# Kernel tuning notes

Hardware: AMD Instinct MI355X
Metric: run time of the kernel (lower is better)

The kernel has to match this reference:

```python
import jax, jax.numpy as jnp
import numpy as np

N_NODES = 100000
N_EDGES = 800000
D_NODE = 64          # node_channels
D_EDGE = 4           # edge_feature_dim (2*layer_idx+2, layer 1)
H_MSG = 128          # message_hidden_channels
H_UPD = 128          # update_hidden_channels


def setup_inputs() -> dict:
    key = jax.random.key(0)
    ks = jax.random.split(key, 9)
    s = 0.05  # small init scale for numerical stability
    return {
        "x": jax.random.normal(ks[0], (N_NODES, D_NODE), dtype=jnp.float32),
        "edge_index": jax.random.randint(ks[1], (2, N_EDGES), 0, N_NODES, dtype=jnp.int32),
        "edge_features": jax.random.uniform(ks[2], (N_EDGES, D_EDGE), dtype=jnp.float32),
        "W1": jax.random.normal(ks[3], (2 * D_NODE + D_EDGE, H_MSG), dtype=jnp.float32) * s,
        "b1": jnp.zeros((H_MSG,), dtype=jnp.float32),
        "W2": jax.random.normal(ks[4], (H_MSG, D_NODE), dtype=jnp.float32) * s,
        "b2": jnp.zeros((D_NODE,), dtype=jnp.float32),
        "U1": jax.random.normal(ks[5], (2 * D_NODE, H_UPD), dtype=jnp.float32) * s,
        "bu1": jnp.zeros((H_UPD,), dtype=jnp.float32),
        "U2": jax.random.normal(ks[6], (H_UPD, D_NODE), dtype=jnp.float32) * s,
        "bu2": jnp.zeros((D_NODE,), dtype=jnp.float32),
    }


def reference(x, edge_index, edge_features, W1, b1, W2, b2, U1, bu1, U2, bu2):
    src, dst = edge_index[0], edge_index[1]
    # message phase: gather endpoints, log1p edge feats, concat, 2-layer MLP
    ef = jnp.log1p(edge_features)                       # [E, D_EDGE]
    msg_in = jnp.concatenate([x[src], x[dst], ef], axis=-1)  # [E, 2D+De]
    messages = jax.nn.relu(msg_in @ W1 + b1) @ W2 + b2  # [E, D_NODE]
    # aggregate: scatter-add into destination nodes
    agg = jnp.zeros_like(x).at[dst].add(messages)       # [N, D_NODE]
    # update phase
    upd_in = jnp.concatenate([x, agg], axis=-1)         # [N, 2*D_NODE]
    return jax.nn.relu(upd_in @ U1 + bu1) @ U2 + bu2    # [N, D_NODE]
```

## Files before the change

### kernel.cpp

```cpp
#include <hip/hip_runtime.h>
#include <math.h>

#define NN 100000
#define NE 800000
#define DN 64
#define DE 4
#define HH 128
#define NT 64
#define NT2 64
#define SCAN_B 256
#define NBLK_SCAN ((NN + SCAN_B - 1) / SCAN_B)
#define EPAD 16
#define AGG_BLOCKS 2048

using bf16x8 = __attribute__((ext_vector_type(8))) short;
using f32x4  = __attribute__((ext_vector_type(4))) float;

__device__ __forceinline__ unsigned short f2bf(float f) {
    unsigned int u = __float_as_uint(f);
    unsigned int r = (u + 0x7fffu + ((u >> 16) & 1u)) >> 16;
    return (unsigned short)r;
}
__device__ __forceinline__ float bf2f(unsigned short h) {
    return __uint_as_float(((unsigned int)h) << 16);
}
__device__ __forceinline__ float2 bfpair2f(unsigned int v) {
    return make_float2(__uint_as_float(v << 16),
                       __uint_as_float(v & 0xffff0000u));
}
__device__ __forceinline__ int rfl_i(int v) { return __builtin_amdgcn_readfirstlane(v); }

__global__ __launch_bounds__(256) void k_xproj(const float* __restrict__ x,
                                               const unsigned short* __restrict__ Wpx,
                                               unsigned short* __restrict__ XAb,
                                               float* __restrict__ XB) {
    __shared__ unsigned short sA[8 * 64 * 8];
    const int n0 = blockIdx.x * NT;
    const int t  = threadIdx.x;
    const int w    = t >> 6;
    const int l    = t & 63;
    const int quad = l >> 4;
    const int l16  = l & 15;

#pragma unroll
    for (int it = 0; it < 4; ++it) {
        const int flat = t + it * 256;
        const int node = flat >> 4;
        const int c    = flat & 15;
        const int gn   = n0 + node;
        float4 v = make_float4(0.f, 0.f, 0.f, 0.f);
        if (gn < NN) v = *(const float4*)(x + (size_t)gn * DN + c * 4);
        const int k = c * 4, Q = k >> 3, j0 = k & 7;
        uint2 pk;
        pk.x = (unsigned)f2bf(v.x) | ((unsigned)f2bf(v.y) << 16);
        pk.y = (unsigned)f2bf(v.z) | ((unsigned)f2bf(v.w) << 16);
        *(uint2*)(&sA[(Q * 64 + node) * 8 + j0]) = pk;
    }
    __syncthreads();

    const int mrow = w * 16 + l16;
    f32x4 acc[16];
#pragma unroll
    for (int nt = 0; nt < 16; ++nt) { acc[nt][0] = 0.f; acc[nt][1] = 0.f; acc[nt][2] = 0.f; acc[nt][3] = 0.f; }

#pragma unroll
    for (int kb = 0; kb < 2; ++kb) {
        bf16x8 a = *(const bf16x8*)(const void*)(&sA[((kb * 4 + quad) * 64 + mrow) * 8]);
#pragma unroll
        for (int nt = 0; nt < 16; ++nt) {
            bf16x8 b = *(const bf16x8*)(const void*)(Wpx + ((size_t)(nt * 2 + kb) * 64 + l) * 8);
            acc[nt] = __builtin_amdgcn_mfma_f32_16x16x32_bf16(a, b, acc[nt], 0, 0, 0);
        }
    }
#pragma unroll
    for (int nt = 0; nt < 8; ++nt) {
        const int col = nt * 16 + l16;
#pragma unroll
        for (int r = 0; r < 4; ++r) {
            const int gn = n0 + w * 16 + quad * 4 + r;
            if (gn < NN) XAb[(size_t)gn * HH + col] = f2bf(acc[nt][r]);
        }
    }
#pragma unroll
    for (int nt = 8; nt < 16; ++nt) {
        const int col = (nt - 8) * 16 + l16;
#pragma unroll
        for (int r = 0; r < 4; ++r) {
            const int gn = n0 + w * 16 + quad * 4 + r;
            if (gn < NN) XB[(size_t)gn * HH + col] = acc[nt][r];
        }
    }
}

__global__ __launch_bounds__(256) void k_fold(const float* __restrict__ W2,
                                              const float* __restrict__ U1,
                                              const float* __restrict__ b2,
                                              float* __restrict__ Wc,
                                              float* __restrict__ cvec) {
    const int idx = blockIdx.x * 256 + threadIdx.x;
    const float* u1b = U1 + (size_t)DN * HH;
    if (blockIdx.x < 64) {
        const int r = idx >> 7;
        const int c = idx & 127;
        float acc = 0.f;
#pragma unroll 8
        for (int j = 0; j < DN; ++j)
            acc = fmaf(W2[(size_t)r * DN + j], u1b[(size_t)j * HH + c], acc);
        Wc[(size_t)r * HH + c] = acc;
    } else if (threadIdx.x < HH) {
        const int c = threadIdx.x;
        float acc = 0.f;
#pragma unroll 8
        for (int j = 0; j < DN; ++j)
            acc = fmaf(b2[j], u1b[(size_t)j * HH + c], acc);
        cvec[c] = acc;
    }
}

__global__ __launch_bounds__(256) void k_pack(const float* __restrict__ U1,
                                              const float* __restrict__ Wc,
                                              const float* __restrict__ U2,
                                              const float* __restrict__ W1,
                                              unsigned short* __restrict__ Wpa,
                                              unsigned short* __restrict__ Wpb,
                                              unsigned short* __restrict__ Wpx) {
    const int tid = blockIdx.x * 256 + threadIdx.x;
    if (tid < 3072) {
        const int l  = tid & 63;
        const int kb = (tid >> 6) % 6;
        const int n  = tid / 384;
        const int kbase = kb * 32 + (l >> 4) * 8;
        const int col   = n * 16 + (l & 15);
        unsigned short tmp[8];
#pragma unroll
        for (int j = 0; j < 8; ++j) {
            const int k = kbase + j;
            const float v = (k < DN) ? U1[(size_t)k * HH + col]
                                     : Wc[(size_t)(k - DN) * HH + col];
            tmp[j] = f2bf(v);
        }
        *(uint4*)(Wpa + (size_t)tid * 8) = *(const uint4*)tmp;
    } else if (tid < 4096) {
        const int t2 = tid - 3072;
        const int l  = t2 & 63;
        const int kb = (t2 >> 6) & 3;
        const int n2 = t2 >> 8;
        const int kbase = kb * 32 + (l >> 4) * 8;
        const int col   = n2 * 16 + (l & 15);
        unsigned short tmp[8];
#pragma unroll
        for (int j = 0; j < 8; ++j) tmp[j] = f2bf(U2[(size_t)(kbase + j) * DN + col]);
        *(uint4*)(Wpb + (size_t)t2 * 8) = *(const uint4*)tmp;
    } else if (tid < 6144) {
        const int t3 = tid - 4096;
        const int l  = t3 & 63;
        const int kb = (t3 >> 6) & 1;
        const int nt = t3 >> 7;
        const int kbase = kb * 32 + (l >> 4) * 8;
        const int row0  = (nt < 8) ? 0 : DN;
        const int col   = ((nt & 7) * 16) + (l & 15);
        unsigned short tmp[8];
#pragma unroll
        for (int j = 0; j < 8; ++j)
            tmp[j] = f2bf(W1[(size_t)(row0 + kbase + j) * HH + col]);
        *(uint4*)(Wpx + (size_t)t3 * 8) = *(const uint4*)tmp;
    }
}

__global__ __launch_bounds__(256) void k_rank(const int* __restrict__ ei,
                                              int* __restrict__ cnt,
                                              unsigned short* __restrict__ rank,
                                              int* __restrict__ es) {
    const int e = blockIdx.x * 256 + threadIdx.x;
    if (e < NE) {
        const int d = ei[NE + e];
        rank[e] = (unsigned short)atomicAdd(&cnt[d], 1);
    }
    if (blockIdx.x == 0 && threadIdx.x < EPAD) es[NE + threadIdx.x] = 0;
}

__global__ __launch_bounds__(SCAN_B) void k_scan_a(const int* __restrict__ cnt,
                                                   int* __restrict__ pos,
                                                   int* __restrict__ bsum) {
    __shared__ int sh[SCAN_B];
    const int n = blockIdx.x * SCAN_B + threadIdx.x;
    const int c = (n < NN) ? cnt[n] : 0;
    sh[threadIdx.x] = c;
    __syncthreads();
    int v = c;
#pragma unroll
    for (int off = 1; off < SCAN_B; off <<= 1) {
        int add = (threadIdx.x >= off) ? sh[threadIdx.x - off] : 0;
        __syncthreads();
        v += add;
        sh[threadIdx.x] = v;
        __syncthreads();
    }
    if (n < NN) pos[n] = v - c;
    if (threadIdx.x == SCAN_B - 1) bsum[blockIdx.x] = v;
}

__global__ __launch_bounds__(512) void k_scan_b(int* __restrict__ bsum) {
    __shared__ int sh[512];
    const int i = threadIdx.x;
    const int c = (i < NBLK_SCAN) ? bsum[i] : 0;
    sh[i] = c;
    __syncthreads();
    int v = c;
#pragma unroll
    for (int off = 1; off < 512; off <<= 1) {
        int add = (i >= off) ? sh[i - off] : 0;
        __syncthreads();
        v += add;
        sh[i] = v;
        __syncthreads();
    }
    if (i < NBLK_SCAN) bsum[i] = v - c;
}

__global__ __launch_bounds__(256) void k_scatter(const int* __restrict__ ei,
                                                 const float* __restrict__ ef,
                                                 const int* __restrict__ pos,
                                                 const int* __restrict__ boff,
                                                 const unsigned short* __restrict__ rank,
                                                 int* __restrict__ es,
                                                 float4* __restrict__ ef4) {
    const int e = blockIdx.x * 256 + threadIdx.x;
    if (e >= NE) return;
    const int s = ei[e];
    const int d = ei[NE + e];
    const int slot = pos[d] + boff[d >> 8] + (int)rank[e];
    es[slot] = s * (HH * 2);
    ef4[slot] = make_float4(log1pf(ef[e * 4 + 0]), log1pf(ef[e * 4 + 1]),
                            log1pf(ef[e * 4 + 2]), log1pf(ef[e * 4 + 3]));
}

#define EDGE_COMPUTE_V(ff, aa)                                   \
    {                                                            \
        const float2 av = bfpair2f(aa);                          \
        float h0 = av.x + base0;                                 \
        float h1 = av.y + base1;                                 \
        h0 = fmaf(ff.x, wv0.x, h0); h0 = fmaf(ff.y, wv1.x, h0);  \
        h0 = fmaf(ff.z, wv2.x, h0); h0 = fmaf(ff.w, wv3.x, h0);  \
        h1 = fmaf(ff.x, wv0.y, h1); h1 = fmaf(ff.y, wv1.y, h1);  \
        h1 = fmaf(ff.z, wv2.y, h1); h1 = fmaf(ff.w, wv3.y, h1);  \
        acc0 += fmaxf(h0, 0.f);                                  \
        acc1 += fmaxf(h1, 0.f);                                  \
    }

__global__ __launch_bounds__(256) void k_agg(const int* __restrict__ es,
                                             const float4* __restrict__ ef4,
                                             const int* __restrict__ pos,
                                             const int* __restrict__ boff,
                                             const int* __restrict__ cnt,
                                             const unsigned short* __restrict__ XAb,
                                             const float* __restrict__ XB,
                                             const float* __restrict__ W1,
                                             const float* __restrict__ b1,
                                             unsigned short* __restrict__ Haggb,
                                             float* __restrict__ deg) {
    const int lane = threadIdx.x & 63;
    const int wid  = rfl_i(blockIdx.x * 4 + (threadIdx.x >> 6));
    const int nw   = AGG_BLOCKS * 4;
    const int j0   = lane * 2;
    const unsigned jb = (unsigned)(lane * 4);
    const char* XAc = (const char*)XAb;

    const float* we = W1 + 128 * HH;
    const float2 bb  = *(const float2*)(b1 + j0);
    const float2 wv0 = *(const float2*)(we + 0 * HH + j0);
    const float2 wv1 = *(const float2*)(we + 1 * HH + j0);
    const float2 wv2 = *(const float2*)(we + 2 * HH + j0);
    const float2 wv3 = *(const float2*)(we + 3 * HH + j0);

    for (int du = wid; du < NN; du += nw) {
        const int c     = rfl_i(cnt[du]);
        const int start = rfl_i(pos[du]) + rfl_i(boff[du >> 8]);
        const int end   = start + c;

        const float2 xb = *(const float2*)(XB + (size_t)du * HH + j0);
        const float base0 = xb.x + bb.x;
        const float base1 = xb.y + bb.y;

        float acc0 = 0.f, acc1 = 0.f;
        if (c > 0) {
            int eA0 = rfl_i(es[start + 0]), eA1 = rfl_i(es[start + 1]);
            int eB0 = rfl_i(es[start + 2]), eB1 = rfl_i(es[start + 3]);
            unsigned aA0 = 0u, aA1 = 0u, aB0 = 0u, aB1 = 0u;
            float4 fA0 = make_float4(0.f, 0.f, 0.f, 0.f);
            float4 fA1 = fA0, fB0 = fA0, fB1 = fA0;
            aA0 = *(const unsigned*)(XAc + (unsigned)eA0 + jb);
            fA0 = ef4[start + 0];
            if (c > 1) { aA1 = *(const unsigned*)(XAc + (unsigned)eA1 + jb); fA1 = ef4[start + 1]; }
            if (c > 2) { aB0 = *(const unsigned*)(XAc + (unsigned)eB0 + jb); fB0 = ef4[start + 2]; }
            if (c > 3) { aB1 = *(const unsigned*)(XAc + (unsigned)eB1 + jb); fB1 = ef4[start + 3]; }
            eA0 = rfl_i(es[start + 4]); eA1 = rfl_i(es[start + 5]);
            eB0 = rfl_i(es[start + 6]); eB1 = rfl_i(es[start + 7]);

            int k = start;
            while (true) {
                EDGE_COMPUTE_V(fA0, aA0);
                if (k + 1 < end) EDGE_COMPUTE_V(fA1, aA1);
                if (k + 2 >= end) break;
                if (k + 4 < end) { aA0 = *(const unsigned*)(XAc + (unsigned)eA0 + jb); fA0 = ef4[k + 4]; }
                if (k + 5 < end) { aA1 = *(const unsigned*)(XAc + (unsigned)eA1 + jb); fA1 = ef4[k + 5]; }
                eA0 = rfl_i(es[k + 8]); eA1 = rfl_i(es[k + 9]);
                EDGE_COMPUTE_V(fB0, aB0);
                if (k + 3 < end) EDGE_COMPUTE_V(fB1, aB1);
                if (k + 4 >= end) break;
                if (k + 6 < end) { aB0 = *(const unsigned*)(XAc + (unsigned)eB0 + jb); fB0 = ef4[k + 6]; }
                if (k + 7 < end) { aB1 = *(const unsigned*)(XAc + (unsigned)eB1 + jb); fB1 = ef4[k + 7]; }
                eB0 = rfl_i(es[k + 10]); eB1 = rfl_i(es[k + 11]);
                k += 4;
            }
        }
        const unsigned int p = (unsigned)f2bf(acc0) | ((unsigned)f2bf(acc1) << 16);
        *(unsigned int*)(Haggb + (size_t)du * HH + j0) = p;
        if (lane == 0) deg[du] = (float)c;
    }
}

__global__ __launch_bounds__(256) void k_edge_atomic(const int* __restrict__ ei,
                                                     const float* __restrict__ ef,
                                                     const float* __restrict__ W1,
                                                     const float* __restrict__ b1,
                                                     const unsigned short* __restrict__ XAb,
                                                     const float* __restrict__ XB,
                                                     float* __restrict__ Hagg,
                                                     float* __restrict__ deg) {
    const int wave = threadIdx.x >> 6;
    const int lane = threadIdx.x & 63;
    const long e = (long)blockIdx.x * 4 + wave;
    if (e >= NE) return;
    const int s = ei[e];
    const int d = ei[NE + e];

    float t = 0.f;
    if (lane < DE) t = log1pf(ef[e * DE + lane]);
    const float l0 = __shfl(t, 0);
    const float l1 = __shfl(t, 1);
    const float l2 = __shfl(t, 2);
    const float l3 = __shfl(t, 3);

    const float* we = W1 + 128 * HH;
    const size_t sb = (size_t)s * HH;
    const size_t db = (size_t)d * HH;
#pragma unroll
    for (int r = 0; r < 2; ++r) {
        const int j = lane + r * 64;
        float h = bf2f(XAb[sb + j]) + XB[db + j] + b1[j];
        h = fmaf(l0, we[0 * HH + j], h);
        h = fmaf(l1, we[1 * HH + j], h);
        h = fmaf(l2, we[2 * HH + j], h);
        h = fmaf(l3, we[3 * HH + j], h);
        h = fmaxf(h, 0.f);
        atomicAdd(&Hagg[db + j], h);
    }
    if (lane == 0) atomicAdd(&deg[d], 1.f);
}

__global__ __launch_bounds__(256) void k_update(const float* __restrict__ x,
                                                const void* __restrict__ HaggV,
                                                const int hbf16,
                                                const float* __restrict__ deg,
                                                const unsigned short* __restrict__ Wpa,
                                                const unsigned short* __restrict__ Wpb,
                                                const float* __restrict__ cvec,
                                                const float* __restrict__ bu1,
                                                const float* __restrict__ bu2,
                                                float* __restrict__ out) {
    __shared__ unsigned short sA[6 * 4 * 64 * 8];
    __shared__ float sdeg[NT2];
    const int n0 = blockIdx.x * NT2;
    const int t  = threadIdx.x;
    const int w    = t >> 6;
    const int l    = t & 63;
    const int quad = l >> 4;
    const int l16  = l & 15;

#pragma unroll
    for (int it = 0; it < 4; ++it) {
        const int flat = t + it * 256;
        const int node = flat >> 4;
        const int c    = flat & 15;
        const int gn   = n0 + node;
        float4 v = make_float4(0.f, 0.f, 0.f, 0.f);
        if (gn < NN) v = *(const float4*)(x + (size_t)gn * DN + c * 4);
        const int k = c * 4, Q = k >> 3, j0 = k & 7;
        uint2 pk;
        pk.x = (unsigned)f2bf(v.x) | ((unsigned)f2bf(v.y) << 16);
        pk.y = (unsigned)f2bf(v.z) | ((unsigned)f2bf(v.w) << 16);
        *(uint2*)(&sA[(Q * 64 + node) * 8 + j0]) = pk;
    }
    if (hbf16) {
        const unsigned short* Hb = (const unsigned short*)HaggV;
#pragma unroll
        for (int it = 0; it < 4; ++it) {
            const int flat = t + it * 256;
            const int node = flat >> 4;
            const int c8   = flat & 15;
            const int gn   = n0 + node;
            uint4 v = make_uint4(0u, 0u, 0u, 0u);
            if (gn < NN) v = *(const uint4*)(Hb + (size_t)gn * HH + c8 * 8);
            const int Q = 8 + c8;
            *(uint4*)(&sA[(Q * 64 + node) * 8]) = v;
        }
    } else {
        const float* Hagg = (const float*)HaggV;
#pragma unroll
        for (int it = 0; it < 8; ++it) {
            const int flat = t + it * 256;
            const int node = flat >> 5;
            const int c    = flat & 31;
            const int gn   = n0 + node;
            float4 v = make_float4(0.f, 0.f, 0.f, 0.f);
            if (gn < NN) v = *(const float4*)(Hagg + (size_t)gn * HH + c * 4);
            const int k = DN + c * 4, Q = k >> 3, j0 = k & 7;
            uint2 pk;
            pk.x = (unsigned)f2bf(v.x) | ((unsigned)f2bf(v.y) << 16);
            pk.y = (unsigned)f2bf(v.z) | ((unsigned)f2bf(v.w) << 16);
            *(uint2*)(&sA[(Q * 64 + node) * 8 + j0]) = pk;
        }
    }
    if (t < NT2) sdeg[t] = (n0 + t < NN) ? deg[n0 + t] : 0.f;
    __syncthreads();

    f32x4 acc[8];
#pragma unroll
    for (int n = 0; n < 8; ++n) {
        const int col = n * 16 + l16;
        const float bv = bu1[col];
        const float cv = cvec[col];
#pragma unroll
        for (int r = 0; r < 4; ++r)
            acc[n][r] = fmaf(sdeg[w * 16 + quad * 4 + r], cv, bv);
    }
    const int mrow = w * 16 + l16;
#pragma unroll
    for (int kb = 0; kb < 6; ++kb) {
        bf16x8 a = *(const bf16x8*)(const void*)(&sA[((kb * 4 + quad) * 64 + mrow) * 8]);
#pragma unroll
        for (int n = 0; n < 8; ++n) {
            bf16x8 b = *(const bf16x8*)(const void*)(Wpa + ((size_t)(n * 6 + kb) * 64 + l) * 8);
            acc[n] = __builtin_amdgcn_mfma_f32_16x16x32_bf16(a, b, acc[n], 0, 0, 0);
        }
    }
    __syncthreads();

#pragma unroll
    for (int n = 0; n < 8; ++n) {
        const int col = n * 16 + l16;
        const int Q = col >> 3;
        const int j = col & 7;
#pragma unroll
        for (int r = 0; r < 4; ++r) {
            const int m = w * 16 + quad * 4 + r;
            sA[(Q * 64 + m) * 8 + j] = f2bf(fmaxf(acc[n][r], 0.f));
        }
    }
    __syncthreads();

    f32x4 acc2[4];
#pragma unroll
    for (int n2 = 0; n2 < 4; ++n2) {
        const float bv = bu2[n2 * 16 + l16];
        acc2[n2][0] = bv; acc2[n2][1] = bv; acc2[n2][2] = bv; acc2[n2][3] = bv;
    }
#pragma unroll
    for (int kb = 0; kb < 4; ++kb) {
        bf16x8 a = *(const bf16x8*)(const void*)(&sA[((kb * 4 + quad) * 64 + mrow) * 8]);
#pragma unroll
        for (int n2 = 0; n2 < 4; ++n2) {
            bf16x8 b = *(const bf16x8*)(const void*)(Wpb + ((size_t)(n2 * 4 + kb) * 64 + l) * 8);
            acc2[n2] = __builtin_amdgcn_mfma_f32_16x16x32_bf16(a, b, acc2[n2], 0, 0, 0);
        }
    }
#pragma unroll
    for (int n2 = 0; n2 < 4; ++n2) {
        const int col = n2 * 16 + l16;
#pragma unroll
        for (int r = 0; r < 4; ++r) {
            const int gn = n0 + w * 16 + quad * 4 + r;
            if (gn < NN) out[(size_t)gn * DN + col] = acc2[n2][r];
        }
    }
}

extern "C" void kernel_launch(void* const* d_in, const int* in_sizes, int n_in,
                              void* d_out, int out_size, void* d_ws, size_t ws_size,
                              hipStream_t stream) {
    const float* x   = (const float*)d_in[0];
    const int*   ei  = (const int*)d_in[1];
    const float* ef  = (const float*)d_in[2];
    const float* W1  = (const float*)d_in[3];
    const float* b1  = (const float*)d_in[4];
    const float* W2  = (const float*)d_in[5];
    const float* b2  = (const float*)d_in[6];
    const float* U1  = (const float*)d_in[7];
    const float* bu1 = (const float*)d_in[8];
    const float* U2  = (const float*)d_in[9];
    const float* bu2 = (const float*)d_in[10];
    float* out = (float*)d_out;

    unsigned short* XAb = (unsigned short*)d_ws;
    float* XB   = (float*)(XAb + (size_t)NN * HH);
    float* Hagg = XB + (size_t)NN * HH;
    float* deg  = Hagg + (size_t)NN * HH;
    float* Wc   = deg + NN;
    float* cvec = Wc + (size_t)HH * HH;
    unsigned short* Wpa = (unsigned short*)(cvec + HH);
    unsigned short* Wpb = Wpa + 8 * 6 * 64 * 8;
    unsigned short* Wpx = Wpb + 4 * 4 * 64 * 8;
    int*   cnt  = (int*)(Wpx + 16 * 2 * 64 * 8);
    int*   pos  = cnt + NN;
    int*   boff = pos + NN;
    int*   es   = boff + 1024;
    float4* ef4 = (float4*)(es + NE + EPAD);
    unsigned short* rank = (unsigned short*)(ef4 + NE + EPAD);
    const size_t need = (size_t)((char*)(rank + NE) - (char*)d_ws);

    unsigned short* Haggb = (unsigned short*)Hagg;

    const int nblk  = (NN + NT - 1) / NT;
    const int nblk2 = (NN + NT2 - 1) / NT2;

    k_fold<<<65, 256, 0, stream>>>(W2, U1, b2, Wc, cvec);
    k_pack<<<24, 256, 0, stream>>>(U1, Wc, U2, W1, Wpa, Wpb, Wpx);

    if (ws_size >= need) {
        hipMemsetAsync(cnt, 0, (size_t)NN * sizeof(int), stream);
        k_xproj<<<nblk, 256, 0, stream>>>(x, Wpx, XAb, XB);
        k_rank<<<(NE + 255) / 256, 256, 0, stream>>>(ei, cnt, rank, es);
        k_scan_a<<<NBLK_SCAN, SCAN_B, 0, stream>>>(cnt, pos, boff);
        k_scan_b<<<1, 512, 0, stream>>>(boff);
        k_scatter<<<(NE + 255) / 256, 256, 0, stream>>>(ei, ef, pos, boff, rank, es, ef4);
        k_agg<<<AGG_BLOCKS, 256, 0, stream>>>(es, ef4, pos, boff, cnt, XAb, XB, W1, b1, Haggb, deg);
        k_update<<<nblk2, 256, 0, stream>>>(x, (const void*)Haggb, 1, deg, Wpa, Wpb, cvec, bu1, bu2, out);
    } else {
        hipMemsetAsync(Hagg, 0, ((size_t)NN * HH + NN) * sizeof(float), stream);
        k_xproj<<<nblk, 256, 0, stream>>>(x, Wpx, XAb, XB);
        k_edge_atomic<<<NE / 4, 256, 0, stream>>>(ei, ef, W1, b1, XAb, XB, Hagg, deg);
        k_update<<<nblk2, 256, 0, stream>>>(x, (const void*)Hagg, 0, deg, Wpa, Wpb, cvec, bu1, bu2, out);
    }
}
```

Baseline: 271.6 us.

## Fuse CSR edge aggregation into update MLP kernel via shared memory

Merges the per-destination edge aggregation kernel with the update MLP kernel. Each 64-node block now gathers its own incoming edges, accumulates the hidden activations, and writes them as bf16 straight into the shared-memory A tile used by the MFMA update GEMMs. This removes the global write and re-read of the bf16 Hagg buffer and one kernel launch. In exchange the gather loses the grid-stride load balancing of the old 2048-block kernel, and it shares occupancy and register pressure with the MFMA stage, which may hurt latency hiding on the irregular gathers.

```diff
diff --git a/kernel.cpp b/kernel.cpp
--- a/kernel.cpp
+++ b/kernel.cpp
@@ -11,7 +11,6 @@
 #define SCAN_B 256
 #define NBLK_SCAN ((NN + SCAN_B - 1) / SCAN_B)
 #define EPAD 16
-#define AGG_BLOCKS 2048
 
 using bf16x8 = __attribute__((ext_vector_type(8))) short;
 using f32x4  = __attribute__((ext_vector_type(4))) float;
@@ -248,75 +247,167 @@
         acc1 += fmaxf(h1, 0.f);                                  \
     }
 
-__global__ __launch_bounds__(256) void k_agg(const int* __restrict__ es,
-                                             const float4* __restrict__ ef4,
-                                             const int* __restrict__ pos,
-                                             const int* __restrict__ boff,
-                                             const int* __restrict__ cnt,
-                                             const unsigned short* __restrict__ XAb,
-                                             const float* __restrict__ XB,
-                                             const float* __restrict__ W1,
-                                             const float* __restrict__ b1,
-                                             unsigned short* __restrict__ Haggb,
-                                             float* __restrict__ deg) {
-    const int lane = threadIdx.x & 63;
-    const int wid  = rfl_i(blockIdx.x * 4 + (threadIdx.x >> 6));
-    const int nw   = AGG_BLOCKS * 4;
-    const int j0   = lane * 2;
-    const unsigned jb = (unsigned)(lane * 4);
-    const char* XAc = (const char*)XAb;
-
-    const float* we = W1 + 128 * HH;
-    const float2 bb  = *(const float2*)(b1 + j0);
-    const float2 wv0 = *(const float2*)(we + 0 * HH + j0);
-    const float2 wv1 = *(const float2*)(we + 1 * HH + j0);
-    const float2 wv2 = *(const float2*)(we + 2 * HH + j0);
-    const float2 wv3 = *(const float2*)(we + 3 * HH + j0);
-
-    for (int du = wid; du < NN; du += nw) {
-        const int c     = rfl_i(cnt[du]);
-        const int start = rfl_i(pos[du]) + rfl_i(boff[du >> 8]);
-        const int end   = start + c;
-
-        const float2 xb = *(const float2*)(XB + (size_t)du * HH + j0);
-        const float base0 = xb.x + bb.x;
-        const float base1 = xb.y + bb.y;
-
-        float acc0 = 0.f, acc1 = 0.f;
-        if (c > 0) {
-            int eA0 = rfl_i(es[start + 0]), eA1 = rfl_i(es[start + 1]);
-            int eB0 = rfl_i(es[start + 2]), eB1 = rfl_i(es[start + 3]);
-            unsigned aA0 = 0u, aA1 = 0u, aB0 = 0u, aB1 = 0u;
-            float4 fA0 = make_float4(0.f, 0.f, 0.f, 0.f);
-            float4 fA1 = fA0, fB0 = fA0, fB1 = fA0;
-            aA0 = *(const unsigned*)(XAc + (unsigned)eA0 + jb);
-            fA0 = ef4[start + 0];
-            if (c > 1) { aA1 = *(const unsigned*)(XAc + (unsigned)eA1 + jb); fA1 = ef4[start + 1]; }
-            if (c > 2) { aB0 = *(const unsigned*)(XAc + (unsigned)eB0 + jb); fB0 = ef4[start + 2]; }
-            if (c > 3) { aB1 = *(const unsigned*)(XAc + (unsigned)eB1 + jb); fB1 = ef4[start + 3]; }
-            eA0 = rfl_i(es[start + 4]); eA1 = rfl_i(es[start + 5]);
-            eB0 = rfl_i(es[start + 6]); eB1 = rfl_i(es[start + 7]);
-
-            int k = start;
-            while (true) {
-                EDGE_COMPUTE_V(fA0, aA0);
-                if (k + 1 < end) EDGE_COMPUTE_V(fA1, aA1);
-                if (k + 2 >= end) break;
-                if (k + 4 < end) { aA0 = *(const unsigned*)(XAc + (unsigned)eA0 + jb); fA0 = ef4[k + 4]; }
-                if (k + 5 < end) { aA1 = *(const unsigned*)(XAc + (unsigned)eA1 + jb); fA1 = ef4[k + 5]; }
-                eA0 = rfl_i(es[k + 8]); eA1 = rfl_i(es[k + 9]);
-                EDGE_COMPUTE_V(fB0, aB0);
-                if (k + 3 < end) EDGE_COMPUTE_V(fB1, aB1);
-                if (k + 4 >= end) break;
-                if (k + 6 < end) { aB0 = *(const unsigned*)(XAc + (unsigned)eB0 + jb); fB0 = ef4[k + 6]; }
-                if (k + 7 < end) { aB1 = *(const unsigned*)(XAc + (unsigned)eB1 + jb); fB1 = ef4[k + 7]; }
-                eB0 = rfl_i(es[k + 10]); eB1 = rfl_i(es[k + 11]);
-                k += 4;
+__global__ __launch_bounds__(256) void k_upd_fused(const int* __restrict__ es,
+                                                   const float4* __restrict__ ef4,
+                                                   const int* __restrict__ pos,
+                                                   const int* __restrict__ boff,
+                                                   const int* __restrict__ cnt,
+                                                   const unsigned short* __restrict__ XAb,
+                                                   const float* __restrict__ XB,
+                                                   const float* __restrict__ W1,
+                                                   const float* __restrict__ b1,
+                                                   const float* __restrict__ x,
+                                                   const unsigned short* __restrict__ Wpa,
+                                                   const unsigned short* __restrict__ Wpb,
+                                                   const float* __restrict__ cvec,
+                                                   const float* __restrict__ bu1,
+                                                   const float* __restrict__ bu2,
+                                                   float* __restrict__ out) {
+    __shared__ unsigned short sA[6 * 4 * 64 * 8];
+    __shared__ float sdeg[NT2];
+    const int n0 = blockIdx.x * NT2;
+    const int t  = threadIdx.x;
+    const int w    = t >> 6;
+    const int l    = t & 63;
+    const int quad = l >> 4;
+    const int l16  = l & 15;
+
+#pragma unroll
+    for (int it = 0; it < 4; ++it) {
+        const int flat = t + it * 256;
+        const int node = flat >> 4;
+        const int c    = flat & 15;
+        const int gn   = n0 + node;
+        float4 v = make_float4(0.f, 0.f, 0.f, 0.f);
+        if (gn < NN) v = *(const float4*)(x + (size_t)gn * DN + c * 4);
+        const int k = c * 4, Q = k >> 3, j0 = k & 7;
+        uint2 pk;
+        pk.x = (unsigned)f2bf(v.x) | ((unsigned)f2bf(v.y) << 16);
+        pk.y = (unsigned)f2bf(v.z) | ((unsigned)f2bf(v.w) << 16);
+        *(uint2*)(&sA[(Q * 64 + node) * 8 + j0]) = pk;
+    }
+    if (t < NT2) sdeg[t] = (n0 + t < NN) ? (float)cnt[n0 + t] : 0.f;
+
+    {
+        const int j0 = l * 2;
+        const unsigned jb = (unsigned)(l * 4);
+        const char* XAc = (const char*)XAb;
+        const float* we = W1 + 128 * HH;
+        const float2 bb  = *(const float2*)(b1 + j0);
+        const float2 wv0 = *(const float2*)(we + 0 * HH + j0);
+        const float2 wv1 = *(const float2*)(we + 1 * HH + j0);
+        const float2 wv2 = *(const float2*)(we + 2 * HH + j0);
+        const float2 wv3 = *(const float2*)(we + 3 * HH + j0);
+        const int Qh = 8 + (l >> 2);
+        const int jh = j0 & 7;
+
+        for (int i = 0; i < 16; ++i) {
+            const int node = w * 16 + i;
+            const int du = n0 + node;
+            float acc0 = 0.f, acc1 = 0.f;
+            if (du < NN) {
+                const int c     = rfl_i(cnt[du]);
+                const int start = rfl_i(pos[du]) + rfl_i(boff[du >> 8]);
+                const int end   = start + c;
+                const float2 xb = *(const float2*)(XB + (size_t)du * HH + j0);
+                const float base0 = xb.x + bb.x;
+                const float base1 = xb.y + bb.y;
+                if (c > 0) {
+                    int eA0 = rfl_i(es[start + 0]), eA1 = rfl_i(es[start + 1]);
+                    int eB0 = rfl_i(es[start + 2]), eB1 = rfl_i(es[start + 3]);
+                    unsigned aA0 = 0u, aA1 = 0u, aB0 = 0u, aB1 = 0u;
+                    float4 fA0 = make_float4(0.f, 0.f, 0.f, 0.f);
+                    float4 fA1 = fA0, fB0 = fA0, fB1 = fA0;
+                    aA0 = *(const unsigned*)(XAc + (unsigned)eA0 + jb);
+                    fA0 = ef4[start + 0];
+                    if (c > 1) { aA1 = *(const unsigned*)(XAc + (unsigned)eA1 + jb); fA1 = ef4[start + 1]; }
+                    if (c > 2) { aB0 = *(const unsigned*)(XAc + (unsigned)eB0 + jb); fB0 = ef4[start + 2]; }
+                    if (c > 3) { aB1 = *(const unsigned*)(XAc + (unsigned)eB1 + jb); fB1 = ef4[start + 3]; }
+                    eA0 = rfl_i(es[start + 4]); eA1 = rfl_i(es[start + 5]);
+                    eB0 = rfl_i(es[start + 6]); eB1 = rfl_i(es[start + 7]);
+
+                    int k = start;
+                    while (true) {
+                        EDGE_COMPUTE_V(fA0, aA0);
+                        if (k + 1 < end) EDGE_COMPUTE_V(fA1, aA1);
+                        if (k + 2 >= end) break;
+                        if (k + 4 < end) { aA0 = *(const unsigned*)(XAc + (unsigned)eA0 + jb); fA0 = ef4[k + 4]; }
+                        if (k + 5 < end) { aA1 = *(const unsigned*)(XAc + (unsigned)eA1 + jb); fA1 = ef4[k + 5]; }
+                        eA0 = rfl_i(es[k + 8]); eA1 = rfl_i(es[k + 9]);
+                        EDGE_COMPUTE_V(fB0, aB0);
+                        if (k + 3 < end) EDGE_COMPUTE_V(fB1, aB1);
+                        if (k + 4 >= end) break;
+                        if (k + 6 < end) { aB0 = *(const unsigned*)(XAc + (unsigned)eB0 + jb); fB0 = ef4[k + 6]; }
+                        if (k + 7 < end) { aB1 = *(const unsigned*)(XAc + (unsigned)eB1 + jb); fB1 = ef4[k + 7]; }
+                        eB0 = rfl_i(es[k + 10]); eB1 = rfl_i(es[k + 11]);
+                        k += 4;
+                    }
+                }
             }
-        }
-        const unsigned int p = (unsigned)f2bf(acc0) | ((unsigned)f2bf(acc1) << 16);
-        *(unsigned int*)(Haggb + (size_t)du * HH + j0) = p;
-        if (lane == 0) deg[du] = (float)c;
+            const unsigned p = (unsigned)f2bf(acc0) | ((unsigned)f2bf(acc1) << 16);
+            *(unsigned*)(&sA[(Qh * 64 + node) * 8 + jh]) = p;
+        }
+    }
+    __syncthreads();
+
+    f32x4 acc[8];
+#pragma unroll
+    for (int n = 0; n < 8; ++n) {
+        const int col = n * 16 + l16;
+        const float bv = bu1[col];
+        const float cv = cvec[col];
+#pragma unroll
+        for (int r = 0; r < 4; ++r)
+            acc[n][r] = fmaf(sdeg[w * 16 + quad * 4 + r], cv, bv);
+    }
+    const int mrow = w * 16 + l16;
+#pragma unroll
+    for (int kb = 0; kb < 6; ++kb) {
+        bf16x8 a = *(const bf16x8*)(const void*)(&sA[((kb * 4 + quad) * 64 + mrow) * 8]);
+#pragma unroll
+        for (int n = 0; n < 8; ++n) {
+            bf16x8 b = *(const bf16x8*)(const void*)(Wpa + ((size_t)(n * 6 + kb) * 64 + l) * 8);
+            acc[n] = __builtin_amdgcn_mfma_f32_16x16x32_bf16(a, b, acc[n], 0, 0, 0);
+        }
+    }
+    __syncthreads();
+
+#pragma unroll
+    for (int n = 0; n < 8; ++n) {
+        const int col = n * 16 + l16;
+        const int Q = col >> 3;
+        const int j = col & 7;
+#pragma unroll
+        for (int r = 0; r < 4; ++r) {
+            const int m = w * 16 + quad * 4 + r;
+            sA[(Q * 64 + m) * 8 + j] = f2bf(fmaxf(acc[n][r], 0.f));
+        }
+    }
+    __syncthreads();
+
+    f32x4 acc2[4];
+#pragma unroll
+    for (int n2 = 0; n2 < 4; ++n2) {
+        const float bv = bu2[n2 * 16 + l16];
+        acc2[n2][0] = bv; acc2[n2][1] = bv; acc2[n2][2] = bv; acc2[n2][3] = bv;
+    }
+#pragma unroll
+    for (int kb = 0; kb < 4; ++kb) {
+        bf16x8 a = *(const bf16x8*)(const void*)(&sA[((kb * 4 + quad) * 64 + mrow) * 8]);
+#pragma unroll
+        for (int n2 = 0; n2 < 4; ++n2) {
+            bf16x8 b = *(const bf16x8*)(const void*)(Wpb + ((size_t)(n2 * 4 + kb) * 64 + l) * 8);
+            acc2[n2] = __builtin_amdgcn_mfma_f32_16x16x32_bf16(a, b, acc2[n2], 0, 0, 0);
+        }
+    }
+#pragma unroll
+    for (int n2 = 0; n2 < 4; ++n2) {
+        const int col = n2 * 16 + l16;
+#pragma unroll
+        for (int r = 0; r < 4; ++r) {
+            const int gn = n0 + w * 16 + quad * 4 + r;
+            if (gn < NN) out[(size_t)gn * DN + col] = acc2[n2][r];
+        }
     }
 }
 
@@ -360,8 +451,7 @@
 }
 
 __global__ __launch_bounds__(256) void k_update(const float* __restrict__ x,
-                                                const void* __restrict__ HaggV,
-                                                const int hbf16,
+                                                const float* __restrict__ Hagg,
                                                 const float* __restrict__ deg,
                                                 const unsigned short* __restrict__ Wpa,
                                                 const unsigned short* __restrict__ Wpb,
@@ -392,35 +482,19 @@
         pk.y = (unsigned)f2bf(v.z) | ((unsigned)f2bf(v.w) << 16);
         *(uint2*)(&sA[(Q * 64 + node) * 8 + j0]) = pk;
     }
-    if (hbf16) {
-        const unsigned short* Hb = (const unsigned short*)HaggV;
-#pragma unroll
-        for (int it = 0; it < 4; ++it) {
-            const int flat = t + it * 256;
-            const int node = flat >> 4;
-            const int c8   = flat & 15;
-            const int gn   = n0 + node;
-            uint4 v = make_uint4(0u, 0u, 0u, 0u);
-            if (gn < NN) v = *(const uint4*)(Hb + (size_t)gn * HH + c8 * 8);
-            const int Q = 8 + c8;
-            *(uint4*)(&sA[(Q * 64 + node) * 8]) = v;
-        }
-    } else {
-        const float* Hagg = (const float*)HaggV;
-#pragma unroll
-        for (int it = 0; it < 8; ++it) {
-            const int flat = t + it * 256;
-            const int node = flat >> 5;
-            const int c    = flat & 31;
-            const int gn   = n0 + node;
-            float4 v = make_float4(0.f, 0.f, 0.f, 0.f);
-            if (gn < NN) v = *(const float4*)(Hagg + (size_t)gn * HH + c * 4);
-            const int k = DN + c * 4, Q = k >> 3, j0 = k & 7;
-            uint2 pk;
-            pk.x = (unsigned)f2bf(v.x) | ((unsigned)f2bf(v.y) << 16);
-            pk.y = (unsigned)f2bf(v.z) | ((unsigned)f2bf(v.w) << 16);
-            *(uint2*)(&sA[(Q * 64 + node) * 8 + j0]) = pk;
-        }
+#pragma unroll
+    for (int it = 0; it < 8; ++it) {
+        const int flat = t + it * 256;
+        const int node = flat >> 5;
+        const int c    = flat & 31;
+        const int gn   = n0 + node;
+        float4 v = make_float4(0.f, 0.f, 0.f, 0.f);
+        if (gn < NN) v = *(const float4*)(Hagg + (size_t)gn * HH + c * 4);
+        const int k = DN + c * 4, Q = k >> 3, j0 = k & 7;
+        uint2 pk;
+        pk.x = (unsigned)f2bf(v.x) | ((unsigned)f2bf(v.y) << 16);
+        pk.y = (unsigned)f2bf(v.z) | ((unsigned)f2bf(v.w) << 16);
+        *(uint2*)(&sA[(Q * 64 + node) * 8 + j0]) = pk;
     }
     if (t < NT2) sdeg[t] = (n0 + t < NN) ? deg[n0 + t] : 0.f;
     __syncthreads();
@@ -519,8 +593,6 @@
     unsigned short* rank = (unsigned short*)(ef4 + NE + EPAD);
     const size_t need = (size_t)((char*)(rank + NE) - (char*)d_ws);
 
-    unsigned short* Haggb = (unsigned short*)Hagg;
-
     const int nblk  = (NN + NT - 1) / NT;
     const int nblk2 = (NN + NT2 - 1) / NT2;
 
@@ -534,12 +606,12 @@
         k_scan_a<<<NBLK_SCAN, SCAN_B, 0, stream>>>(cnt, pos, boff);
         k_scan_b<<<1, 512, 0, stream>>>(boff);
         k_scatter<<<(NE + 255) / 256, 256, 0, stream>>>(ei, ef, pos, boff, rank, es, ef4);
-        k_agg<<<AGG_BLOCKS, 256, 0, stream>>>(es, ef4, pos, boff, cnt, XAb, XB, W1, b1, Haggb, deg);
-        k_update<<<nblk2, 256, 0, stream>>>(x, (const void*)Haggb, 1, deg, Wpa, Wpb, cvec, bu1, bu2, out);
+        k_upd_fused<<<nblk2, 256, 0, stream>>>(es, ef4, pos, boff, cnt, XAb, XB, W1, b1,
+                                               x, Wpa, Wpb, cvec, bu1, bu2, out);
     } else {
         hipMemsetAsync(Hagg, 0, ((size_t)NN * HH + NN) * sizeof(float), stream);
         k_xproj<<<nblk, 256, 0, stream>>>(x, Wpx, XAb, XB);
         k_edge_atomic<<<NE / 4, 256, 0, stream>>>(ei, ef, W1, b1, XAb, XB, Hagg, deg);
-        k_update<<<nblk2, 256, 0, stream>>>(x, (const void*)Hagg, 0, deg, Wpa, Wpb, cvec, bu1, bu2, out);
-    }
-}
+        k_update<<<nblk2, 256, 0, stream>>>(x, Hagg, deg, Wpa, Wpb, cvec, bu1, bu2, out);
+    }
+}
```

Result: slower. 280.0 us (+3.1%).
